# Kernel tuning notes

Measured on AMD Instinct MI355X. Metric: run time of the kernel, lower is better.

Reference implementation:

```python
import jax, jax.numpy as jnp
import numpy as np

B, T = 2, 4096
TOK_DIM, POS_DIM = 64, 64
N_HEADS, HEAD_DIM = 8, 32
D_MODEL = 256


def setup_inputs() -> dict:
    key = jax.random.key(0)
    ks = jax.random.split(key, 5)
    s = 0.02
    return {
        "x": jax.random.normal(ks[0], (B, T, TOK_DIM + POS_DIM), dtype=jnp.float32),
        "Wq": jax.random.normal(ks[1], (POS_DIM, N_HEADS * HEAD_DIM), dtype=jnp.float32) * s,
        "Wk": jax.random.normal(ks[2], (POS_DIM, N_HEADS * HEAD_DIM), dtype=jnp.float32) * s,
        "Wv": jax.random.normal(ks[3], (TOK_DIM, N_HEADS * HEAD_DIM), dtype=jnp.float32) * s,
        "Wo": jax.random.normal(ks[4], (N_HEADS * HEAD_DIM, D_MODEL), dtype=jnp.float32) * s,
    }


def reference(x, Wq, Wk, Wv, Wo):
    Bb, Tt, _ = x.shape
    x_tok = x[:, :, :TOK_DIM]   # V comes from token dims
    x_pos = x[:, :, TOK_DIM:]   # Q,K come from positional dims

    # [B, T, H, Dh] -> [B, H, T, Dh]
    q = (x_pos @ Wq).reshape(Bb, Tt, N_HEADS, HEAD_DIM).transpose(0, 2, 1, 3)
    k = (x_pos @ Wk).reshape(Bb, Tt, N_HEADS, HEAD_DIM).transpose(0, 2, 1, 3)
    v = (x_tok @ Wv).reshape(Bb, Tt, N_HEADS, HEAD_DIM).transpose(0, 2, 1, 3)

    scale = 1.0 / jnp.sqrt(jnp.float32(HEAD_DIM))
    scores = jnp.einsum("bhqd,bhkd->bhqk", q, k) * scale  # [B,H,T,T]
    causal = jnp.tril(jnp.ones((Tt, Tt), dtype=bool))
    scores = jnp.where(causal[None, None, :, :], scores, -jnp.inf)
    attn = jax.nn.softmax(scores, axis=-1)

    out = jnp.einsum("bhqk,bhkd->bhqd", attn, v)          # [B,H,T,Dh]
    out = out.transpose(0, 2, 1, 3).reshape(Bb, Tt, N_HEADS * HEAD_DIM)
    return out @ Wo
```

## Files before the change

### kernel.cpp

```cpp
#include <hip/hip_runtime.h>

typedef __attribute__((ext_vector_type(8))) short bf16x8;
typedef __attribute__((ext_vector_type(4))) float f32x4;
typedef __attribute__((ext_vector_type(16))) float f32x16;

#define NB 2
#define SEQ 4096
#define NHD 8
#define HDIM 32
#define DMODEL 256

#define QSCALE 0.25503506f

__device__ __forceinline__ short f2bf(float f) {
  union { float f; unsigned u; } v; v.f = f;
  unsigned r = v.u + 0x7fffu + ((v.u >> 16) & 1u);
  return (short)(r >> 16);
}

__global__ __launch_bounds__(256) void proj_kernel(
    const float* __restrict__ x, const float* __restrict__ Wq,
    const float* __restrict__ Wk, const float* __restrict__ Wv,
    const float* __restrict__ Wo,
    short* __restrict__ Q, short* __restrict__ K, short* __restrict__ VT,
    short* __restrict__ WoT)
{
  __shared__ float xs[8][128];
  const int tid = threadIdx.x;
  const int row0 = blockIdx.x * 8;
  {
    const float4* src = (const float4*)(x + (size_t)row0 * 128);
    float4* dst = (float4*)xs;
    dst[tid] = src[tid];
  }
  if (blockIdx.x < 256)
    WoT[blockIdx.x * 256 + tid] = f2bf(Wo[tid * 256 + blockIdx.x]);
  __syncthreads();
  const int c = tid;
  float qa[8], ka[8], va[8];
#pragma unroll
  for (int r = 0; r < 8; ++r) { qa[r] = 0.f; ka[r] = 0.f; va[r] = 0.f; }
  for (int d4 = 0; d4 < 16; ++d4) {
    float wq[4], wk[4], wv[4];
#pragma unroll
    for (int j = 0; j < 4; ++j) {
      const int d = d4 * 4 + j;
      wq[j] = Wq[d * 256 + c];
      wk[j] = Wk[d * 256 + c];
      wv[j] = Wv[d * 256 + c];
    }
#pragma unroll
    for (int r = 0; r < 8; ++r) {
      const float4 xt = *(const float4*)&xs[r][d4 * 4];
      const float4 xp = *(const float4*)&xs[r][64 + d4 * 4];
      qa[r] += xp.x * wq[0] + xp.y * wq[1] + xp.z * wq[2] + xp.w * wq[3];
      ka[r] += xp.x * wk[0] + xp.y * wk[1] + xp.z * wk[2] + xp.w * wk[3];
      va[r] += xt.x * wv[0] + xt.y * wv[1] + xt.z * wv[2] + xt.w * wv[3];
    }
  }
  const int b = row0 >> 12;
  const int t0 = row0 & 4095;
  const int h = c >> 5, d = c & 31;
  const int bh = b * NHD + h;
#pragma unroll
  for (int r = 0; r < 8; ++r) {
    const int row = t0 + r;
    Q[(bh * SEQ + row) * HDIM + d] = f2bf(qa[r] * QSCALE);
    const int prow = (row & ~31) | (row & 19) | ((row & 4) << 1) | ((row & 8) >> 1);
    K[(bh * SEQ + prow) * HDIM + d] = f2bf(ka[r]);
  }
  bf16x8 vv;
#pragma unroll
  for (int r = 0; r < 8; ++r) vv[r] = f2bf(va[r]);
  *(bf16x8*)&VT[(size_t)(bh * HDIM + d) * SEQ + t0] = vv;
}

template <bool MASKED>
__device__ __forceinline__ void score_to_p(const f32x16& S, int hi, int l31,
                                           float& lsum, bf16x8& p0v, bf16x8& p1v)
{
  union { unsigned u[4]; bf16x8 v; } p0, p1;
#pragma unroll
  for (int i = 0; i < 8; ++i) {
    const int r0 = 2 * i;
    float e0, e1;
    if (MASKED) {
      const int koff = (r0 & 3) + (((r0 >> 2) & 1) << 2) + (((r0 >> 3) & 1) << 4) + (hi << 3);
      e0 = (koff     <= l31) ? __builtin_amdgcn_exp2f(S[r0])     : 0.f;
      e1 = (koff + 1 <= l31) ? __builtin_amdgcn_exp2f(S[r0 + 1]) : 0.f;
    } else {
      e0 = __builtin_amdgcn_exp2f(S[r0]);
      e1 = __builtin_amdgcn_exp2f(S[r0 + 1]);
    }
    lsum += e0 + e1;
    unsigned wd;
    asm("v_cvt_pk_bf16_f32 %0, %1, %2" : "=v"(wd) : "v"(e0), "v"(e1));
    if (i < 4) p0.u[i] = wd; else p1.u[i - 4] = wd;
  }
  p0v = p0.v; p1v = p1.v;
}

__global__ __launch_bounds__(256, 4) void attn_kernel(
    const short* __restrict__ Q, const short* __restrict__ K,
    const short* __restrict__ VT, short* __restrict__ O)
{
  __shared__ float MG[8][17][64];

  const int flat = blockIdx.x;
  const int bh = (flat & 7) + (((flat >> 3) & 1) << 3);
  const int p = flat >> 4;
  const int tA = p, tB = 127 - p;
  const int q0A = tA << 5, q0B = tB << 5;
  const int ncA = tA + 1, ncB = tB + 1;

  const int w = threadIdx.x >> 6;
  const int lane = threadIdx.x & 63;
  const int l31 = lane & 31;
  const int hi = lane >> 5;

  const short* Kb  = K  + (size_t)bh * SEQ * HDIM;
  const short* VTb = VT + (size_t)bh * HDIM * SEQ;

  const short* qrowA = &Q[((size_t)bh * SEQ + q0A + l31) * HDIM + hi * 8];
  const bf16x8 qfA0 = *(const bf16x8*)qrowA;
  const bf16x8 qfA1 = *(const bf16x8*)(qrowA + 16);
  const short* qrowB = &Q[((size_t)bh * SEQ + q0B + l31) * HDIM + hi * 8];
  const bf16x8 qfB0 = *(const bf16x8*)qrowB;
  const bf16x8 qfB1 = *(const bf16x8*)(qrowB + 16);

  const f32x16 z16 = {0.f,0.f,0.f,0.f,0.f,0.f,0.f,0.f,0.f,0.f,0.f,0.f,0.f,0.f,0.f,0.f};
  f32x16 accA = z16, accB = z16;
  float lsumA = 0.f, lsumB = 0.f;

  int c = w;
  bf16x8 kf0, kf1, vf0, vf1;
  {
    const int kb = c << 5;
    const short* krow = &Kb[(size_t)(kb + l31) * HDIM + hi * 8];
    kf0 = *(const bf16x8*)krow;
    kf1 = *(const bf16x8*)(krow + 16);
    const short* vrow = &VTb[(size_t)l31 * SEQ + kb + hi * 8];
    vf0 = *(const bf16x8*)vrow;
    vf1 = *(const bf16x8*)(vrow + 16);
  }

  for (; c < ncA; c += 4) {
    const int kb = c << 5;
    const int cn = c + 4;
    bf16x8 kn0, kn1, vn0, vn1;
    if (cn < ncB) {
      const int kbn = cn << 5;
      const short* krow = &Kb[(size_t)(kbn + l31) * HDIM + hi * 8];
      kn0 = *(const bf16x8*)krow;
      kn1 = *(const bf16x8*)(krow + 16);
      const short* vrow = &VTb[(size_t)l31 * SEQ + kbn + hi * 8];
      vn0 = *(const bf16x8*)vrow;
      vn1 = *(const bf16x8*)(vrow + 16);
    }
    {
      f32x16 S = __builtin_amdgcn_mfma_f32_32x32x16_bf16(kf0, qfB0, z16, 0, 0, 0);
      S = __builtin_amdgcn_mfma_f32_32x32x16_bf16(kf1, qfB1, S, 0, 0, 0);
      bf16x8 p0v, p1v;
      score_to_p<false>(S, hi, l31, lsumB, p0v, p1v);
      accB = __builtin_amdgcn_mfma_f32_32x32x16_bf16(vf0, p0v, accB, 0, 0, 0);
      accB = __builtin_amdgcn_mfma_f32_32x32x16_bf16(vf1, p1v, accB, 0, 0, 0);
    }
    {
      f32x16 S = __builtin_amdgcn_mfma_f32_32x32x16_bf16(kf0, qfA0, z16, 0, 0, 0);
      S = __builtin_amdgcn_mfma_f32_32x32x16_bf16(kf1, qfA1, S, 0, 0, 0);
      bf16x8 p0v, p1v;
      if (kb == q0A) score_to_p<true >(S, hi, l31, lsumA, p0v, p1v);
      else           score_to_p<false>(S, hi, l31, lsumA, p0v, p1v);
      accA = __builtin_amdgcn_mfma_f32_32x32x16_bf16(vf0, p0v, accA, 0, 0, 0);
      accA = __builtin_amdgcn_mfma_f32_32x32x16_bf16(vf1, p1v, accA, 0, 0, 0);
    }
    kf0 = kn0; kf1 = kn1; vf0 = vn0; vf1 = vn1;
  }

  for (; c < ncB; c += 4) {
    const int kb = c << 5;
    const int cn = c + 4;
    bf16x8 kn0, kn1, vn0, vn1;
    if (cn < ncB) {
      const int kbn = cn << 5;
      const short* krow = &Kb[(size_t)(kbn + l31) * HDIM + hi * 8];
      kn0 = *(const bf16x8*)krow;
      kn1 = *(const bf16x8*)(krow + 16);
      const short* vrow = &VTb[(size_t)l31 * SEQ + kbn + hi * 8];
      vn0 = *(const bf16x8*)vrow;
      vn1 = *(const bf16x8*)(vrow + 16);
    }
    f32x16 S = __builtin_amdgcn_mfma_f32_32x32x16_bf16(kf0, qfB0, z16, 0, 0, 0);
    S = __builtin_amdgcn_mfma_f32_32x32x16_bf16(kf1, qfB1, S, 0, 0, 0);
    bf16x8 p0v, p1v;
    if (kb == q0B) score_to_p<true >(S, hi, l31, lsumB, p0v, p1v);
    else           score_to_p<false>(S, hi, l31, lsumB, p0v, p1v);
    accB = __builtin_amdgcn_mfma_f32_32x32x16_bf16(vf0, p0v, accB, 0, 0, 0);
    accB = __builtin_amdgcn_mfma_f32_32x32x16_bf16(vf1, p1v, accB, 0, 0, 0);
    kf0 = kn0; kf1 = kn1; vf0 = vn0; vf1 = vn1;
  }

#pragma unroll
  for (int i = 0; i < 16; ++i) MG[w][i][lane] = accA[i];
  MG[w][16][lane] = lsumA;
#pragma unroll
  for (int i = 0; i < 16; ++i) MG[4 + w][i][lane] = accB[i];
  MG[4 + w][16][lane] = lsumB;
  __syncthreads();
  if (w < 2) {
    const int base = w << 2;
    const int q0 = w ? q0B : q0A;
    float fa[16];
#pragma unroll
    for (int i = 0; i < 16; ++i) fa[i] = 0.f;
    float fl = 0.f;
#pragma unroll
    for (int w2 = 0; w2 < 4; ++w2) {
#pragma unroll
      for (int i = 0; i < 16; ++i) fa[i] += MG[base + w2][i][lane];
      fl += MG[base + w2][16][lane] + MG[base + w2][16][lane ^ 32];
    }
    const float inv = 1.f / fl;
    const size_t obase = ((size_t)bh * SEQ + q0 + l31) * HDIM;
#pragma unroll
    for (int rg = 0; rg < 4; ++rg) {
      const int d0 = (rg << 3) + (hi << 2);
      short4 st;
      st.x = f2bf(fa[rg * 4 + 0] * inv);
      st.y = f2bf(fa[rg * 4 + 1] * inv);
      st.z = f2bf(fa[rg * 4 + 2] * inv);
      st.w = f2bf(fa[rg * 4 + 3] * inv);
      *(short4*)&O[obase + d0] = st;
    }
  }
}

__global__ __launch_bounds__(256) void ogemm_kernel(
    const short* __restrict__ O, const short* __restrict__ WoT, float* __restrict__ out)
{
  const int w = threadIdx.x >> 6;
  const int lane = threadIdx.x & 63;
  const int l15 = lane & 15, g = lane >> 4;
  const int m0 = blockIdx.x * 64 + w * 16;
  const int n0 = blockIdx.y * 32;
  const int b = m0 >> 12;
  const int t = (m0 & 4095) + l15;

  const short* Ab = &O[(((size_t)b * NHD) * SEQ + t) * HDIM + g * 8];
  const short* B0 = &WoT[(n0 + l15) * 256 + g * 8];
  const short* B1 = &WoT[(n0 + 16 + l15) * 256 + g * 8];

  f32x4 acc0 = {0.f, 0.f, 0.f, 0.f}, acc1 = {0.f, 0.f, 0.f, 0.f};
  bf16x8 af = *(const bf16x8*)Ab;
  bf16x8 b0 = *(const bf16x8*)B0;
  bf16x8 b1 = *(const bf16x8*)B1;
#pragma unroll
  for (int ks = 0; ks < 8; ++ks) {
    bf16x8 an, bn0, bn1;
    if (ks < 7) {
      an  = *(const bf16x8*)(Ab + (size_t)(ks + 1) * SEQ * HDIM);
      bn0 = *(const bf16x8*)(B0 + (ks + 1) * 32);
      bn1 = *(const bf16x8*)(B1 + (ks + 1) * 32);
    }
    acc0 = __builtin_amdgcn_mfma_f32_16x16x32_bf16(af, b0, acc0, 0, 0, 0);
    acc1 = __builtin_amdgcn_mfma_f32_16x16x32_bf16(af, b1, acc1, 0, 0, 0);
    af = an; b0 = bn0; b1 = bn1;
  }
#pragma unroll
  for (int r = 0; r < 4; ++r) {
    const size_t ro = (size_t)(m0 + (g << 2) + r) * 256 + n0 + l15;
    out[ro] = acc0[r];
    out[ro + 16] = acc1[r];
  }
}

extern "C" void kernel_launch(void* const* d_in, const int* in_sizes, int n_in,
                              void* d_out, int out_size, void* d_ws, size_t ws_size,
                              hipStream_t stream)
{
  const float* x  = (const float*)d_in[0];
  const float* Wq = (const float*)d_in[1];
  const float* Wk = (const float*)d_in[2];
  const float* Wv = (const float*)d_in[3];
  const float* Wo = (const float*)d_in[4];
  float* out = (float*)d_out;

  short* Q   = (short*)d_ws;
  short* K   = Q + 2097152;
  short* VT  = K + 2097152;
  short* O   = VT + 2097152;
  short* WoT = O + 2097152;

  proj_kernel<<<dim3(1024), dim3(256), 0, stream>>>(x, Wq, Wk, Wv, Wo, Q, K, VT, WoT);
  attn_kernel<<<dim3(1024), dim3(256), 0, stream>>>(Q, K, VT, O);
  ogemm_kernel<<<dim3(128, 8), dim3(256), 0, stream>>>(O, WoT, out);
}
```

Measured before the change: 137.2 us.

## Split attention KV loop across eight waves with tree reduction of partials

```diff
diff --git a/kernel.cpp b/kernel.cpp
--- a/kernel.cpp
+++ b/kernel.cpp
@@ -100,11 +100,11 @@
   p0v = p0.v; p1v = p1.v;
 }
 
-__global__ __launch_bounds__(256, 4) void attn_kernel(
+__global__ __launch_bounds__(512, 8) void attn_kernel(
     const short* __restrict__ Q, const short* __restrict__ K,
     const short* __restrict__ VT, short* __restrict__ O)
 {
-  __shared__ float MG[8][17][64];
+  __shared__ float MG[4][2][17][64];
 
   const int flat = blockIdx.x;
   const int bh = (flat & 7) + (((flat >> 3) & 1) << 3);
@@ -144,9 +144,9 @@
     vf1 = *(const bf16x8*)(vrow + 16);
   }
 
-  for (; c < ncA; c += 4) {
+  for (; c < ncA; c += 8) {
     const int kb = c << 5;
-    const int cn = c + 4;
+    const int cn = c + 8;
     bf16x8 kn0, kn1, vn0, vn1;
     if (cn < ncB) {
       const int kbn = cn << 5;
@@ -177,9 +177,9 @@
     kf0 = kn0; kf1 = kn1; vf0 = vn0; vf1 = vn1;
   }
 
-  for (; c < ncB; c += 4) {
+  for (; c < ncB; c += 8) {
     const int kb = c << 5;
-    const int cn = c + 4;
+    const int cn = c + 8;
     bf16x8 kn0, kn1, vn0, vn1;
     if (cn < ncB) {
       const int kbn = cn << 5;
@@ -200,37 +200,62 @@
     kf0 = kn0; kf1 = kn1; vf0 = vn0; vf1 = vn1;
   }
 
-#pragma unroll
-  for (int i = 0; i < 16; ++i) MG[w][i][lane] = accA[i];
-  MG[w][16][lane] = lsumA;
-#pragma unroll
-  for (int i = 0; i < 16; ++i) MG[4 + w][i][lane] = accB[i];
-  MG[4 + w][16][lane] = lsumB;
+  if (w >= 4) {
+    const int s = w - 4;
+#pragma unroll
+    for (int i = 0; i < 16; ++i) { MG[s][0][i][lane] = accA[i]; MG[s][1][i][lane] = accB[i]; }
+    MG[s][0][16][lane] = lsumA; MG[s][1][16][lane] = lsumB;
+  }
+  __syncthreads();
+  if (w < 4) {
+#pragma unroll
+    for (int i = 0; i < 16; ++i) { accA[i] += MG[w][0][i][lane]; accB[i] += MG[w][1][i][lane]; }
+    lsumA += MG[w][0][16][lane]; lsumB += MG[w][1][16][lane];
+  }
+  __syncthreads();
+  if (w == 2 || w == 3) {
+    const int s = w - 2;
+#pragma unroll
+    for (int i = 0; i < 16; ++i) { MG[s][0][i][lane] = accA[i]; MG[s][1][i][lane] = accB[i]; }
+    MG[s][0][16][lane] = lsumA; MG[s][1][16][lane] = lsumB;
+  }
   __syncthreads();
   if (w < 2) {
-    const int base = w << 2;
-    const int q0 = w ? q0B : q0A;
-    float fa[16];
-#pragma unroll
-    for (int i = 0; i < 16; ++i) fa[i] = 0.f;
-    float fl = 0.f;
-#pragma unroll
-    for (int w2 = 0; w2 < 4; ++w2) {
-#pragma unroll
-      for (int i = 0; i < 16; ++i) fa[i] += MG[base + w2][i][lane];
-      fl += MG[base + w2][16][lane] + MG[base + w2][16][lane ^ 32];
-    }
-    const float inv = 1.f / fl;
-    const size_t obase = ((size_t)bh * SEQ + q0 + l31) * HDIM;
+#pragma unroll
+    for (int i = 0; i < 16; ++i) { accA[i] += MG[w][0][i][lane]; accB[i] += MG[w][1][i][lane]; }
+    lsumA += MG[w][0][16][lane]; lsumB += MG[w][1][16][lane];
+  }
+  __syncthreads();
+  if (w == 1) {
+#pragma unroll
+    for (int i = 0; i < 16; ++i) { MG[2][0][i][lane] = accA[i]; MG[2][1][i][lane] = accB[i]; }
+    MG[2][0][16][lane] = lsumA; MG[2][1][16][lane] = lsumB;
+  }
+  __syncthreads();
+  if (w == 0) {
+#pragma unroll
+    for (int i = 0; i < 16; ++i) { accA[i] += MG[2][0][i][lane]; accB[i] += MG[2][1][i][lane]; }
+    lsumA += MG[2][0][16][lane]; lsumB += MG[2][1][16][lane];
+    const float flA = lsumA + __shfl_xor(lsumA, 32);
+    const float flB = lsumB + __shfl_xor(lsumB, 32);
+    const float invA = 1.f / flA;
+    const float invB = 1.f / flB;
+    const size_t obA = ((size_t)bh * SEQ + q0A + l31) * HDIM;
+    const size_t obB = ((size_t)bh * SEQ + q0B + l31) * HDIM;
 #pragma unroll
     for (int rg = 0; rg < 4; ++rg) {
       const int d0 = (rg << 3) + (hi << 2);
-      short4 st;
-      st.x = f2bf(fa[rg * 4 + 0] * inv);
-      st.y = f2bf(fa[rg * 4 + 1] * inv);
-      st.z = f2bf(fa[rg * 4 + 2] * inv);
-      st.w = f2bf(fa[rg * 4 + 3] * inv);
-      *(short4*)&O[obase + d0] = st;
+      short4 sA, sB;
+      sA.x = f2bf(accA[rg * 4 + 0] * invA);
+      sA.y = f2bf(accA[rg * 4 + 1] * invA);
+      sA.z = f2bf(accA[rg * 4 + 2] * invA);
+      sA.w = f2bf(accA[rg * 4 + 3] * invA);
+      sB.x = f2bf(accB[rg * 4 + 0] * invB);
+      sB.y = f2bf(accB[rg * 4 + 1] * invB);
+      sB.z = f2bf(accB[rg * 4 + 2] * invB);
+      sB.w = f2bf(accB[rg * 4 + 3] * invB);
+      *(short4*)&O[obA + d0] = sA;
+      *(short4*)&O[obB + d0] = sB;
     }
   }
 }
@@ -292,6 +317,6 @@
   short* WoT = O + 2097152;
 
   proj_kernel<<<dim3(1024), dim3(256), 0, stream>>>(x, Wq, Wk, Wv, Wo, Q, K, VT, WoT);
-  attn_kernel<<<dim3(1024), dim3(256), 0, stream>>>(Q, K, VT, O);
+  attn_kernel<<<dim3(1024), dim3(512), 0, stream>>>(Q, K, VT, O);
   ogemm_kernel<<<dim3(128, 8), dim3(256), 0, stream>>>(O, WoT, out);
 }
```

After: 348.7 us. +154.1%, slower.
